# Performance work log

Measured on AMD Instinct MI355X. Metric: run time of the kernel, lower is better.

## Reference

```python
import jax, jax.numpy as jnp
import numpy as np

EPS = 1e-7  # keras K.epsilon()
ROUTINGS = 3


def squash(v, axis=-1):
    s = jnp.sum(v * v, axis=axis, keepdims=True)
    scale = s / (1.0 + s) / jnp.sqrt(s + EPS)
    return scale * v


def setup_inputs() -> dict:
    key = jax.random.key(0)
    k1, k2 = jax.random.split(key)
    B, I, K = 256, 2048, 8   # batch, input_num_capsule, input_dim_capsule
    J, D = 10, 16            # num_capsule, dim_capsule
    inputs = jax.random.normal(k1, (B, I, K), dtype=jnp.float32)
    W = jax.random.normal(k2, (J, I, D, K), dtype=jnp.float32) * 0.05
    return {"inputs": inputs, "W": W}


def reference(inputs, W):
    # inputs: [B, I, K]; W: [J, I, D, K]
    # inputs_hat[b,j,i,d] = W[j,i] @ inputs[b,i]  -> [B, J, I, D]
    u_hat = jnp.einsum('jidk,bik->bjid', W, inputs)
    B, J, I, _ = u_hat.shape
    b = jnp.zeros((B, J, 1, I), dtype=u_hat.dtype)
    outputs = None
    for r in range(ROUTINGS):
        c = jax.nn.softmax(b, axis=1)                       # softmax over output capsules
        s = jnp.einsum('bjqi,bjid->bjqd', c, u_hat)          # [B, J, 1, D]
        outputs = squash(s, axis=-1)
        if r < ROUTINGS - 1:
            b = b + jnp.einsum('bjqd,bjid->bjqi', outputs, u_hat)
    return jnp.squeeze(outputs, axis=2)                      # [B, J, D]
```

## Files before the change

### kernel.cpp

```cpp
#include <hip/hip_runtime.h>
#include <math.h>


#define BB 256
#define II 2048
#define KK 8
#define JJ 10
#define DD 16

typedef __attribute__((ext_vector_type(4))) float f32x4;
typedef __attribute__((ext_vector_type(8))) short short8;

__device__ __forceinline__ short f2bf(float f) {
    union { float f; unsigned u; } v; v.f = f;
    unsigned r = v.u + 0x7FFFu + ((v.u >> 16) & 1u);
    return (short)(r >> 16);
}

__global__ __launch_bounds__(256) void pre_kernel(const float* __restrict__ x,
                                                  const float* __restrict__ W,
                                                  short* __restrict__ xTb,
                                                  short* __restrict__ Wb) {
    __shared__ float4 tile[8 * 66];
    const int t = threadIdx.x;
    const int bid = blockIdx.x;
    if (bid < 1280) {
        const int idx = bid * 256 + t;
        const float4* src = (const float4*)(W + (size_t)idx * 8);
        const float4 a = src[0], b = src[1];
        short8 o;
        o[0] = f2bf(a.x); o[1] = f2bf(a.y); o[2] = f2bf(a.z); o[3] = f2bf(a.w);
        o[4] = f2bf(b.x); o[5] = f2bf(b.y); o[6] = f2bf(b.z); o[7] = f2bf(b.w);
        *(short8*)(Wb + (size_t)idx * 8) = o;
    } else {
        const int bb = bid - 1280;
        const int b0 = (bb >> 8) * 32, i0 = (bb & 255) * 8;
        {
            const int lb = t >> 3, li = t & 7;
            const float4* src = (const float4*)(x + ((b0 + lb) * II + (i0 + li)) * KK);
            tile[li * 66 + lb * 2 + 0] = src[0];
            tile[li * 66 + lb * 2 + 1] = src[1];
        }
        __syncthreads();
        {
            const int ri = t >> 5, rb = t & 31;
            const float4 p0 = tile[ri * 66 + rb * 2 + 0];
            const float4 p1 = tile[ri * 66 + rb * 2 + 1];
            short8 o;
            o[0] = f2bf(p0.x); o[1] = f2bf(p0.y); o[2] = f2bf(p0.z); o[3] = f2bf(p0.w);
            o[4] = f2bf(p1.x); o[5] = f2bf(p1.y); o[6] = f2bf(p1.z); o[7] = f2bf(p1.w);
            *(short8*)(xTb + ((size_t)(i0 + ri) * BB + (b0 + rb)) * KK) = o;
        }
    }
}

#define LBUF 14336

__device__ __forceinline__ void seg_src_dst(int s, int i0, int b0,
                                            const short* __restrict__ xTb,
                                            const short* __restrict__ Wb,
                                            const short** src, int* dst) {
    if (s < 20) {
        const int j = s >> 1, h = s & 1;
        *src = Wb + ((size_t)(j * II + i0) * DD) * KK + h * 512;
        *dst = j * 1024 + h * 512;
    } else {
        const int il = s - 20;
        *src = xTb + ((size_t)(i0 + il) * BB + b0) * KK;
        *dst = 10240 + il * 512;
    }
}

template <int USE_C>
__global__ __launch_bounds__(256) void round_mfma(
    const short* __restrict__ xTb, const short* __restrict__ Wb,
    const float* __restrict__ vT, _Float16* __restrict__ p)
{
    __shared__ short L[2][LBUF];
    const int t = threadIdx.x;
    const int lane = t & 63, wv = t >> 6;
    const int col = lane & 15, q = lane >> 4;
    const int bid = blockIdx.x;
    const int chunk = ((bid >> 5) << 3) | (bid & 7);
    const int ytile = (bid >> 3) & 3;
    const int b0 = ytile * 64;
    const int bl = wv * 16 + col;
    const int i0 = chunk * 16;

    short8 r0[7], r1[7];
#pragma unroll
    for (int n = 0; n < 7; ++n) {
        const int s = wv + n * 4;
        const short* src; int dst;
        seg_src_dst(s, i0, b0, xTb, Wb, &src, &dst);
        r0[n] = *(const short8*)(src + lane * 8);
        seg_src_dst(s, i0 + 8, b0, xTb, Wb, &src, &dst);
        r1[n] = *(const short8*)(src + lane * 8);
    }
#pragma unroll
    for (int n = 0; n < 7; ++n) {
        const int s = wv + n * 4;
        const short* src; int dst;
        seg_src_dst(s, i0, b0, xTb, Wb, &src, &dst);
        *(short8*)(&L[0][dst + lane * 8]) = r0[n];
    }
    __syncthreads();

    f32x4 sfrag[JJ];
#pragma unroll
    for (int j = 0; j < JJ; ++j) sfrag[j] = (f32x4){0.f, 0.f, 0.f, 0.f};

    f32x4 vfrag[JJ];
    if (USE_C) {
#pragma unroll
        for (int j = 0; j < JJ; ++j)
            vfrag[j] = *(const f32x4*)(vT + ((size_t)j * BB + b0 + bl) * DD + q * 4);
    }

#pragma unroll
    for (int sc = 0; sc < 2; ++sc) {
        const short* Lb = L[sc];
        if (USE_C) {
            for (int il = 0; il < 8; ++il) {
                short8 A[JJ], Bf;
                const short8 z = (short8){0, 0, 0, 0, 0, 0, 0, 0};
                Bf = z;
#pragma unroll
                for (int j = 0; j < JJ; ++j) A[j] = z;
                if (q == 0) {
                    Bf = *(const short8*)(&Lb[10240 + il * 512 + bl * 8]);
#pragma unroll
                    for (int j = 0; j < JJ; ++j)
                        A[j] = *(const short8*)(&Lb[j * 1024 + il * 128 + col * 8]);
                }
                f32x4 U[JJ];
#pragma unroll
                for (int j = 0; j < JJ; ++j)
                    U[j] = __builtin_amdgcn_mfma_f32_16x16x32_bf16(
                        A[j], Bf, (f32x4){0.f, 0.f, 0.f, 0.f}, 0, 0, 0);
                float Lg[JJ];
#pragma unroll
                for (int j = 0; j < JJ; ++j)
                    Lg[j] = vfrag[j][0] * U[j][0] + vfrag[j][1] * U[j][1]
                          + vfrag[j][2] * U[j][2] + vfrag[j][3] * U[j][3];
#pragma unroll
                for (int j = 0; j < JJ; ++j) {
                    Lg[j] += __shfl_xor(Lg[j], 16, 64);
                    Lg[j] += __shfl_xor(Lg[j], 32, 64);
                }
                float sum = 0.f;
#pragma unroll
                for (int j = 0; j < JJ; ++j) { Lg[j] = __expf(Lg[j]); sum += Lg[j]; }
                const float inv = __builtin_amdgcn_rcpf(sum);
#pragma unroll
                for (int j = 0; j < JJ; ++j) {
                    const float c = Lg[j] * inv;
#pragma unroll
                    for (int r = 0; r < 4; ++r) sfrag[j][r] += c * U[j][r];
                }
            }
        } else {
#pragma unroll
            for (int s = 0; s < 2; ++s) {
                const int il = s * 4 + q;
                const short8 Bf = *(const short8*)(&Lb[10240 + il * 512 + bl * 8]);
#pragma unroll
                for (int j = 0; j < JJ; ++j) {
                    const short8 A = *(const short8*)(&Lb[j * 1024 + il * 128 + col * 8]);
                    sfrag[j] = __builtin_amdgcn_mfma_f32_16x16x32_bf16(A, Bf, sfrag[j], 0, 0, 0);
                }
            }
        }
        if (sc == 0) {
#pragma unroll
            for (int n = 0; n < 7; ++n) {
                const int s = wv + n * 4;
                const short* src; int dst;
                seg_src_dst(s, i0 + 8, b0, xTb, Wb, &src, &dst);
                *(short8*)(&L[1][dst + lane * 8]) = r1[n];
            }
            __syncthreads();
        }
    }

    _Float16* pp = p + (((size_t)(ytile * 4 + wv) * 128 + chunk) * 5) * 512;
#pragma unroll
    for (int jp = 0; jp < 5; ++jp) {
        union { uint4 u; _Float16 h[8]; } pk;
        pk.h[0] = (_Float16)sfrag[2 * jp][0];
        pk.h[1] = (_Float16)sfrag[2 * jp][1];
        pk.h[2] = (_Float16)sfrag[2 * jp][2];
        pk.h[3] = (_Float16)sfrag[2 * jp][3];
        pk.h[4] = (_Float16)sfrag[2 * jp + 1][0];
        pk.h[5] = (_Float16)sfrag[2 * jp + 1][1];
        pk.h[6] = (_Float16)sfrag[2 * jp + 1][2];
        pk.h[7] = (_Float16)sfrag[2 * jp + 1][3];
        *(uint4*)(pp + (size_t)(jp * 64 + lane) * 8) = pk.u;
    }
}

template <int MODE>
__global__ __launch_bounds__(256) void rs_kernel(const _Float16* __restrict__ p,
                                                 float* __restrict__ vT,
                                                 float* __restrict__ out, float scale) {
    __shared__ float red[256][9];
    const int t = threadIdx.x;
    const int jp = blockIdx.x, bt = blockIdx.y;
    const int eg = t & 63, cg = t >> 6;

    const _Float16* pp = p + (((size_t)bt * 128 + cg * 32) * 5 + jp) * 512 + eg * 8;
    float s[8];
#pragma unroll
    for (int r = 0; r < 8; ++r) s[r] = 0.f;
#pragma unroll 4
    for (int ch = 0; ch < 32; ++ch) {
        union { uint4 u; _Float16 h[8]; } cv;
        cv.u = *(const uint4*)(pp + (size_t)ch * (5 * 512));
#pragma unroll
        for (int r = 0; r < 8; ++r) s[r] += (float)cv.h[r];
    }
#pragma unroll
    for (int r = 0; r < 8; ++r) red[t][r] = s[r];
    __syncthreads();
    if (t < 64) {
        float a[8];
#pragma unroll
        for (int r = 0; r < 8; ++r)
            a[r] = red[t][r] + red[t + 64][r] + red[t + 128][r] + red[t + 192][r];
        const int qd = t >> 4, bc = t & 15;
#pragma unroll
        for (int jj = 0; jj < 2; ++jj) {
            const int j = jp * 2 + jj;
            const float x0 = a[jj * 4 + 0] * scale, x1 = a[jj * 4 + 1] * scale;
            const float x2 = a[jj * 4 + 2] * scale, x3 = a[jj * 4 + 3] * scale;
            float ss = x0 * x0 + x1 * x1 + x2 * x2 + x3 * x3;
            ss += __shfl_xor(ss, 16, 64);
            ss += __shfl_xor(ss, 32, 64);
            const float coef = ss / (1.f + ss) / sqrtf(ss + 1e-7f);
            f32x4 v = {coef * x0, coef * x1, coef * x2, coef * x3};
            if (MODE == 0)
                *(f32x4*)(vT + ((size_t)j * BB + bt * 16 + bc) * DD + qd * 4) = v;
            if (MODE == 1) {
                f32x4 o = *(f32x4*)(vT + ((size_t)j * BB + bt * 16 + bc) * DD + qd * 4);
                o += v;
                *(f32x4*)(vT + ((size_t)j * BB + bt * 16 + bc) * DD + qd * 4) = o;
            }
            if (MODE == 2)
                *(f32x4*)(out + ((size_t)(bt * 16 + bc) * JJ + j) * DD + qd * 4) = v;
        }
    }
}

#define IT_OLD 32
#define BT_OLD 16

__global__ __launch_bounds__(256) void zero_kernel(float* __restrict__ p, int n) {
    int idx = blockIdx.x * blockDim.x + threadIdx.x;
    if (idx < n) p[idx] = 0.f;
}

__global__ __launch_bounds__(256) void squash_old(float* __restrict__ s_acc,
                                                  float* __restrict__ dst, float scale,
                                                  int add_to_dst, int zero_src) {
    int idx = blockIdx.x * blockDim.x + threadIdx.x;
    if (idx >= BB * JJ) return;
    float s[DD];
    float ss = 0.f;
#pragma unroll
    for (int d = 0; d < DD; ++d) {
        s[d] = s_acc[idx * DD + d] * scale;
        ss += s[d] * s[d];
    }
    const float coef = ss / (1.f + ss) / sqrtf(ss + 1e-7f);
#pragma unroll
    for (int d = 0; d < DD; ++d) {
        const float vv = coef * s[d];
        if (add_to_dst) dst[idx * DD + d] += vv;
        else            dst[idx * DD + d] = vv;
        if (zero_src)   s_acc[idx * DD + d] = 0.f;
    }
}

__global__ __launch_bounds__(256) void round1_old(const float* __restrict__ x,
                                                  const float* __restrict__ W,
                                                  float* __restrict__ s_acc) {
    const int t = threadIdx.x;
    const int d = t & 15;
    const int bq = t >> 4;
    const int b = blockIdx.y * BT_OLD + bq;
    const int i0 = blockIdx.x * IT_OLD;
    float acc[JJ];
#pragma unroll
    for (int j = 0; j < JJ; ++j) acc[j] = 0.f;
    for (int ii = 0; ii < IT_OLD; ++ii) {
        const int i = i0 + ii;
        const float* xp = x + ((b * II) + i) * KK;
        const float4 xa = *(const float4*)(xp);
        const float4 xb = *(const float4*)(xp + 4);
#pragma unroll
        for (int j = 0; j < JJ; ++j) {
            const float* wp = W + (((j * II + i) * DD + d) * KK);
            const float4 w0 = *(const float4*)(wp);
            const float4 w1 = *(const float4*)(wp + 4);
            acc[j] += w0.x*xa.x + w0.y*xa.y + w0.z*xa.z + w0.w*xa.w
                    + w1.x*xb.x + w1.y*xb.y + w1.z*xb.z + w1.w*xb.w;
        }
    }
#pragma unroll
    for (int j = 0; j < JJ; ++j)
        atomicAdd(&s_acc[(b * JJ + j) * DD + d], acc[j]);
}

__global__ __launch_bounds__(256) void round_old(const float* __restrict__ x,
                                                 const float* __restrict__ W,
                                                 const float* __restrict__ v,
                                                 float* __restrict__ s_acc) {
    const int t = threadIdx.x;
    const int d = t & 15;
    const int bq = t >> 4;
    const int b = blockIdx.y * BT_OLD + bq;
    const int i0 = blockIdx.x * IT_OLD;
    float vr[JJ], acc[JJ];
#pragma unroll
    for (int j = 0; j < JJ; ++j) {
        vr[j] = v[(b * JJ + j) * DD + d];
        acc[j] = 0.f;
    }
    for (int ii = 0; ii < IT_OLD; ++ii) {
        const int i = i0 + ii;
        const float* xp = x + ((b * II) + i) * KK;
        const float4 xa = *(const float4*)(xp);
        const float4 xb = *(const float4*)(xp + 4);
        float U[JJ], Lg[JJ];
#pragma unroll
        for (int j = 0; j < JJ; ++j) {
            const float* wp = W + (((j * II + i) * DD + d) * KK);
            const float4 w0 = *(const float4*)(wp);
            const float4 w1 = *(const float4*)(wp + 4);
            U[j] = w0.x*xa.x + w0.y*xa.y + w0.z*xa.z + w0.w*xa.w
                 + w1.x*xb.x + w1.y*xb.y + w1.z*xb.z + w1.w*xb.w;
            Lg[j] = vr[j] * U[j];
        }
#pragma unroll
        for (int m = 8; m >= 1; m >>= 1) {
#pragma unroll
            for (int j = 0; j < JJ; ++j) Lg[j] += __shfl_xor(Lg[j], m, 64);
        }
        float mx = Lg[0];
#pragma unroll
        for (int j = 1; j < JJ; ++j) mx = fmaxf(mx, Lg[j]);
        float sum = 0.f;
#pragma unroll
        for (int j = 0; j < JJ; ++j) { Lg[j] = __expf(Lg[j] - mx); sum += Lg[j]; }
        const float inv = 1.f / sum;
#pragma unroll
        for (int j = 0; j < JJ; ++j) acc[j] += (Lg[j] * inv) * U[j];
    }
#pragma unroll
    for (int j = 0; j < JJ; ++j)
        atomicAdd(&s_acc[(b * JJ + j) * DD + d], acc[j]);
}

extern "C" void kernel_launch(void* const* d_in, const int* in_sizes, int n_in,
                              void* d_out, int out_size, void* d_ws, size_t ws_size,
                              hipStream_t stream) {
    const float* x = (const float*)d_in[0];
    const float* W = (const float*)d_in[1];
    float* out = (float*)d_out;

    float* vT     = (float*)d_ws;
    _Float16* p   = (_Float16*)(vT + BB * JJ * DD);
    short* xTb    = (short*)(p + (size_t)16 * 128 * 2560);
    short* Wb     = xTb + (size_t)II * BB * KK;
    const size_t need = (size_t)(BB * JJ * DD) * 4
                      + (size_t)16 * 128 * 2560 * 2
                      + ((size_t)II * BB * KK + (size_t)JJ * II * DD * KK) * 2;

    if (ws_size >= need) {
        pre_kernel<<<1280 + 2048, 256, 0, stream>>>(x, W, xTb, Wb);

        dim3 sg(5, 16);
        round_mfma<0><<<512, 256, 0, stream>>>(xTb, Wb, vT, p);
        rs_kernel<0><<<sg, 256, 0, stream>>>(p, vT, out, 0.1f);
        round_mfma<1><<<512, 256, 0, stream>>>(xTb, Wb, vT, p);
        rs_kernel<1><<<sg, 256, 0, stream>>>(p, vT, out, 1.0f);
        round_mfma<1><<<512, 256, 0, stream>>>(xTb, Wb, vT, p);
        rs_kernel<2><<<sg, 256, 0, stream>>>(p, vT, out, 1.0f);
    } else {
        float* s_acc = (float*)d_ws;
        float* v_buf = s_acc + BB * JJ * DD;
        const int NS = BB * JJ * DD;
        dim3 rg(II / IT_OLD, BB / BT_OLD);
        zero_kernel<<<(NS + 255) / 256, 256, 0, stream>>>(s_acc, NS);
        round1_old<<<rg, 256, 0, stream>>>(x, W, s_acc);
        squash_old<<<(BB * JJ + 255) / 256, 256, 0, stream>>>(s_acc, v_buf, 0.1f, 0, 1);
        round_old<<<rg, 256, 0, stream>>>(x, W, v_buf, s_acc);
        squash_old<<<(BB * JJ + 255) / 256, 256, 0, stream>>>(s_acc, v_buf, 1.0f, 1, 1);
        round_old<<<rg, 256, 0, stream>>>(x, W, v_buf, s_acc);
        squash_old<<<(BB * JJ + 255) / 256, 256, 0, stream>>>(s_acc, out, 1.0f, 0, 0);
    }
}
```

Baseline: 146.2 us.

## Fuse preprocessing and all routing rounds into one cooperative kernel with grid syncs

Replaces the seven separate launches (bf16 conversion, three MFMA routing rounds, three reduce/squash passes) with a single cooperative kernel of 512 blocks that uses grid.sync between phases. The goal is to remove launch gaps and kernel-boundary drains between the short dependent stages. In exchange it needs all 512 blocks co-resident, which is why launch_bounds asks for 2 blocks per CU. The reduce/squash phase runs on only 80 blocks while the rest wait at the barrier, and the block-to-tile mapping changes from the swizzled layout. If the cooperative launch fails, the code falls back to the old multi-kernel path.

```diff
diff --git a/kernel.cpp b/kernel.cpp
--- a/kernel.cpp
+++ b/kernel.cpp
@@ -1,5 +1,8 @@
 #include <hip/hip_runtime.h>
+#include <hip/hip_cooperative_groups.h>
 #include <math.h>
+
+namespace cg = cooperative_groups;
 
 
 #define BB 256
@@ -16,6 +19,261 @@
     unsigned r = v.u + 0x7FFFu + ((v.u >> 16) & 1u);
     return (short)(r >> 16);
 }
+
+#define LBUF 14336
+
+__device__ __forceinline__ void seg_src_dst(int s, int i0, int b0,
+                                            const short* __restrict__ xTb,
+                                            const short* __restrict__ Wb,
+                                            const short** src, int* dst) {
+    if (s < 20) {
+        const int j = s >> 1, h = s & 1;
+        *src = Wb + ((size_t)(j * II + i0) * DD) * KK + h * 512;
+        *dst = j * 1024 + h * 512;
+    } else {
+        const int il = s - 20;
+        *src = xTb + ((size_t)(i0 + il) * BB + b0) * KK;
+        *dst = 10240 + il * 512;
+    }
+}
+
+__global__ __launch_bounds__(256, 2) void fused_all(
+    const float* __restrict__ x, const float* __restrict__ W,
+    short* __restrict__ xTb, short* __restrict__ Wb,
+    float* __restrict__ vT, _Float16* __restrict__ p, float* __restrict__ out)
+{
+    __shared__ short L[2][LBUF];
+    cg::grid_group grid = cg::this_grid();
+    const int t = threadIdx.x;
+    const int bid = blockIdx.x;
+
+    for (int u = bid; u < 3328; u += 512) {
+        if (u < 1280) {
+            const int idx = u * 256 + t;
+            const float4* src = (const float4*)(W + (size_t)idx * 8);
+            const float4 a = src[0], b = src[1];
+            short8 o;
+            o[0] = f2bf(a.x); o[1] = f2bf(a.y); o[2] = f2bf(a.z); o[3] = f2bf(a.w);
+            o[4] = f2bf(b.x); o[5] = f2bf(b.y); o[6] = f2bf(b.z); o[7] = f2bf(b.w);
+            *(short8*)(Wb + (size_t)idx * 8) = o;
+        } else {
+            float4* tile = (float4*)(&L[0][0]);
+            const int bb = u - 1280;
+            const int b0p = (bb >> 8) * 32, i0p = (bb & 255) * 8;
+            __syncthreads();
+            {
+                const int lb = t >> 3, li = t & 7;
+                const float4* src = (const float4*)(x + ((b0p + lb) * II + (i0p + li)) * KK);
+                tile[li * 66 + lb * 2 + 0] = src[0];
+                tile[li * 66 + lb * 2 + 1] = src[1];
+            }
+            __syncthreads();
+            {
+                const int ri = t >> 5, rb = t & 31;
+                const float4 p0 = tile[ri * 66 + rb * 2 + 0];
+                const float4 p1 = tile[ri * 66 + rb * 2 + 1];
+                short8 o;
+                o[0] = f2bf(p0.x); o[1] = f2bf(p0.y); o[2] = f2bf(p0.z); o[3] = f2bf(p0.w);
+                o[4] = f2bf(p1.x); o[5] = f2bf(p1.y); o[6] = f2bf(p1.z); o[7] = f2bf(p1.w);
+                *(short8*)(xTb + ((size_t)(i0p + ri) * BB + (b0p + rb)) * KK) = o;
+            }
+        }
+    }
+    grid.sync();
+
+    const int lane = t & 63, wv = t >> 6;
+    const int col = lane & 15, q = lane >> 4;
+    const int chunk = bid & 127;
+    const int ytile = (bid >> 7) & 3;
+    const int b0 = ytile * 64;
+    const int bl = wv * 16 + col;
+    const int i0 = chunk * 16;
+
+    short8 r0[7], r1[7];
+#pragma unroll
+    for (int n = 0; n < 7; ++n) {
+        const int s = wv + n * 4;
+        const short* src; int dst;
+        seg_src_dst(s, i0, b0, xTb, Wb, &src, &dst);
+        r0[n] = *(const short8*)(src + lane * 8);
+        seg_src_dst(s, i0 + 8, b0, xTb, Wb, &src, &dst);
+        r1[n] = *(const short8*)(src + lane * 8);
+    }
+#pragma unroll
+    for (int n = 0; n < 7; ++n) {
+        const int s = wv + n * 4;
+        const short* src; int dst;
+        seg_src_dst(s, i0, b0, xTb, Wb, &src, &dst);
+        *(short8*)(&L[0][dst + lane * 8]) = r0[n];
+    }
+    __syncthreads();
+
+#pragma unroll 1
+    for (int r = 0; r < 3; ++r) {
+        f32x4 sfrag[JJ];
+#pragma unroll
+        for (int j = 0; j < JJ; ++j) sfrag[j] = (f32x4){0.f, 0.f, 0.f, 0.f};
+
+        f32x4 vfrag[JJ];
+        if (r > 0) {
+#pragma unroll
+            for (int j = 0; j < JJ; ++j)
+                vfrag[j] = *(const f32x4*)(vT + ((size_t)j * BB + b0 + bl) * DD + q * 4);
+        }
+
+#pragma unroll
+        for (int sc = 0; sc < 2; ++sc) {
+            const short* Lb = L[sc];
+            if (r > 0) {
+                for (int il = 0; il < 8; ++il) {
+                    short8 A[JJ], Bf;
+                    const short8 z = (short8){0, 0, 0, 0, 0, 0, 0, 0};
+                    Bf = z;
+#pragma unroll
+                    for (int j = 0; j < JJ; ++j) A[j] = z;
+                    if (q == 0) {
+                        Bf = *(const short8*)(&Lb[10240 + il * 512 + bl * 8]);
+#pragma unroll
+                        for (int j = 0; j < JJ; ++j)
+                            A[j] = *(const short8*)(&Lb[j * 1024 + il * 128 + col * 8]);
+                    }
+                    f32x4 U[JJ];
+#pragma unroll
+                    for (int j = 0; j < JJ; ++j)
+                        U[j] = __builtin_amdgcn_mfma_f32_16x16x32_bf16(
+                            A[j], Bf, (f32x4){0.f, 0.f, 0.f, 0.f}, 0, 0, 0);
+                    float Lg[JJ];
+#pragma unroll
+                    for (int j = 0; j < JJ; ++j)
+                        Lg[j] = vfrag[j][0] * U[j][0] + vfrag[j][1] * U[j][1]
+                              + vfrag[j][2] * U[j][2] + vfrag[j][3] * U[j][3];
+#pragma unroll
+                    for (int j = 0; j < JJ; ++j) {
+                        Lg[j] += __shfl_xor(Lg[j], 16, 64);
+                        Lg[j] += __shfl_xor(Lg[j], 32, 64);
+                    }
+                    float sum = 0.f;
+#pragma unroll
+                    for (int j = 0; j < JJ; ++j) { Lg[j] = __expf(Lg[j]); sum += Lg[j]; }
+                    const float inv = __builtin_amdgcn_rcpf(sum);
+#pragma unroll
+                    for (int j = 0; j < JJ; ++j) {
+                        const float c = Lg[j] * inv;
+#pragma unroll
+                        for (int rr = 0; rr < 4; ++rr) sfrag[j][rr] += c * U[j][rr];
+                    }
+                }
+            } else {
+#pragma unroll
+                for (int s = 0; s < 2; ++s) {
+                    const int il = s * 4 + q;
+                    const short8 Bf = *(const short8*)(&Lb[10240 + il * 512 + bl * 8]);
+#pragma unroll
+                    for (int j = 0; j < JJ; ++j) {
+                        const short8 A = *(const short8*)(&Lb[j * 1024 + il * 128 + col * 8]);
+                        sfrag[j] = __builtin_amdgcn_mfma_f32_16x16x32_bf16(A, Bf, sfrag[j], 0, 0, 0);
+                    }
+                }
+            }
+            if (sc == 0) {
+#pragma unroll
+                for (int n = 0; n < 7; ++n) {
+                    const int s = wv + n * 4;
+                    const short* src; int dst;
+                    seg_src_dst(s, i0 + 8, b0, xTb, Wb, &src, &dst);
+                    *(short8*)(&L[1][dst + lane * 8]) = r1[n];
+                }
+                __syncthreads();
+            }
+        }
+
+        _Float16* pp = p + (((size_t)(ytile * 4 + wv) * 128 + chunk) * 5) * 512;
+#pragma unroll
+        for (int jp = 0; jp < 5; ++jp) {
+            union { uint4 u; _Float16 h[8]; } pk;
+            pk.h[0] = (_Float16)sfrag[2 * jp][0];
+            pk.h[1] = (_Float16)sfrag[2 * jp][1];
+            pk.h[2] = (_Float16)sfrag[2 * jp][2];
+            pk.h[3] = (_Float16)sfrag[2 * jp][3];
+            pk.h[4] = (_Float16)sfrag[2 * jp + 1][0];
+            pk.h[5] = (_Float16)sfrag[2 * jp + 1][1];
+            pk.h[6] = (_Float16)sfrag[2 * jp + 1][2];
+            pk.h[7] = (_Float16)sfrag[2 * jp + 1][3];
+            *(uint4*)(pp + (size_t)(jp * 64 + lane) * 8) = pk.u;
+        }
+
+        if (r < 2) {
+#pragma unroll
+            for (int n = 0; n < 7; ++n) {
+                const int s = wv + n * 4;
+                const short* src; int dst;
+                seg_src_dst(s, i0, b0, xTb, Wb, &src, &dst);
+                r0[n] = *(const short8*)(src + lane * 8);
+                seg_src_dst(s, i0 + 8, b0, xTb, Wb, &src, &dst);
+                r1[n] = *(const short8*)(src + lane * 8);
+            }
+#pragma unroll
+            for (int n = 0; n < 7; ++n) {
+                const int s = wv + n * 4;
+                const short* src; int dst;
+                seg_src_dst(s, i0, b0, xTb, Wb, &src, &dst);
+                *(short8*)(&L[0][dst + lane * 8]) = r0[n];
+            }
+        }
+
+        grid.sync();
+
+        if (bid < 80) {
+            const int jp = bid % 5, btq = bid / 5;
+            const int eg = t & 63, cgi = t >> 6;
+            float (*red)[9] = (float (*)[9])(&L[1][0]);
+            const _Float16* prd = p + (((size_t)btq * 128 + cgi * 32) * 5 + jp) * 512 + eg * 8;
+            float sacc[8];
+#pragma unroll
+            for (int rr = 0; rr < 8; ++rr) sacc[rr] = 0.f;
+#pragma unroll 4
+            for (int ch = 0; ch < 32; ++ch) {
+                union { uint4 u; _Float16 h[8]; } cv;
+                cv.u = *(const uint4*)(prd + (size_t)ch * (5 * 512));
+#pragma unroll
+                for (int rr = 0; rr < 8; ++rr) sacc[rr] += (float)cv.h[rr];
+            }
+#pragma unroll
+            for (int rr = 0; rr < 8; ++rr) red[t][rr] = sacc[rr];
+            __syncthreads();
+            if (t < 64) {
+                float a[8];
+#pragma unroll
+                for (int rr = 0; rr < 8; ++rr)
+                    a[rr] = red[t][rr] + red[t + 64][rr] + red[t + 128][rr] + red[t + 192][rr];
+                const int qd = t >> 4, bc = t & 15;
+                const float scale = (r == 0) ? 0.1f : 1.0f;
+#pragma unroll
+                for (int jj = 0; jj < 2; ++jj) {
+                    const int j = jp * 2 + jj;
+                    const float x0 = a[jj * 4 + 0] * scale, x1 = a[jj * 4 + 1] * scale;
+                    const float x2 = a[jj * 4 + 2] * scale, x3 = a[jj * 4 + 3] * scale;
+                    float ss = x0 * x0 + x1 * x1 + x2 * x2 + x3 * x3;
+                    ss += __shfl_xor(ss, 16, 64);
+                    ss += __shfl_xor(ss, 32, 64);
+                    const float coef = ss / (1.f + ss) / sqrtf(ss + 1e-7f);
+                    f32x4 v = {coef * x0, coef * x1, coef * x2, coef * x3};
+                    if (r == 0)
+                        *(f32x4*)(vT + ((size_t)j * BB + btq * 16 + bc) * DD + qd * 4) = v;
+                    else if (r == 1) {
+                        f32x4 o = *(f32x4*)(vT + ((size_t)j * BB + btq * 16 + bc) * DD + qd * 4);
+                        o += v;
+                        *(f32x4*)(vT + ((size_t)j * BB + btq * 16 + bc) * DD + qd * 4) = o;
+                    } else
+                        *(f32x4*)(out + ((size_t)(btq * 16 + bc) * JJ + j) * DD + qd * 4) = v;
+                }
+            }
+        }
+
+        if (r < 2) grid.sync();
+    }
+}
+
 
 __global__ __launch_bounds__(256) void pre_kernel(const float* __restrict__ x,
                                                   const float* __restrict__ W,
@@ -54,23 +312,6 @@
     }
 }
 
-#define LBUF 14336
-
-__device__ __forceinline__ void seg_src_dst(int s, int i0, int b0,
-                                            const short* __restrict__ xTb,
-                                            const short* __restrict__ Wb,
-                                            const short** src, int* dst) {
-    if (s < 20) {
-        const int j = s >> 1, h = s & 1;
-        *src = Wb + ((size_t)(j * II + i0) * DD) * KK + h * 512;
-        *dst = j * 1024 + h * 512;
-    } else {
-        const int il = s - 20;
-        *src = xTb + ((size_t)(i0 + il) * BB + b0) * KK;
-        *dst = 10240 + il * 512;
-    }
-}
-
 template <int USE_C>
 __global__ __launch_bounds__(256) void round_mfma(
     const short* __restrict__ xTb, const short* __restrict__ Wb,
@@ -80,9 +321,8 @@
     const int t = threadIdx.x;
     const int lane = t & 63, wv = t >> 6;
     const int col = lane & 15, q = lane >> 4;
-    const int bid = blockIdx.x;
-    const int chunk = ((bid >> 5) << 3) | (bid & 7);
-    const int ytile = (bid >> 3) & 3;
+    const int chunk = blockIdx.x;
+    const int ytile = blockIdx.y;
     const int b0 = ytile * 64;
     const int bl = wv * 16 + col;
     const int i0 = chunk * 16;
@@ -156,7 +396,7 @@
                 for (int j = 0; j < JJ; ++j) {
                     const float c = Lg[j] * inv;
 #pragma unroll
-                    for (int r = 0; r < 4; ++r) sfrag[j][r] += c * U[j][r];
+                    for (int rr = 0; rr < 4; ++rr) sfrag[j][rr] += c * U[j][rr];
                 }
             }
         } else {
@@ -206,27 +446,27 @@
     __shared__ float red[256][9];
     const int t = threadIdx.x;
     const int jp = blockIdx.x, bt = blockIdx.y;
-    const int eg = t & 63, cg = t >> 6;
-
-    const _Float16* pp = p + (((size_t)bt * 128 + cg * 32) * 5 + jp) * 512 + eg * 8;
+    const int eg = t & 63, cgi = t >> 6;
+
+    const _Float16* pp = p + (((size_t)bt * 128 + cgi * 32) * 5 + jp) * 512 + eg * 8;
     float s[8];
 #pragma unroll
-    for (int r = 0; r < 8; ++r) s[r] = 0.f;
+    for (int rr = 0; rr < 8; ++rr) s[rr] = 0.f;
 #pragma unroll 4
     for (int ch = 0; ch < 32; ++ch) {
         union { uint4 u; _Float16 h[8]; } cv;
         cv.u = *(const uint4*)(pp + (size_t)ch * (5 * 512));
 #pragma unroll
-        for (int r = 0; r < 8; ++r) s[r] += (float)cv.h[r];
-    }
-#pragma unroll
-    for (int r = 0; r < 8; ++r) red[t][r] = s[r];
+        for (int rr = 0; rr < 8; ++rr) s[rr] += (float)cv.h[rr];
+    }
+#pragma unroll
+    for (int rr = 0; rr < 8; ++rr) red[t][rr] = s[rr];
     __syncthreads();
     if (t < 64) {
         float a[8];
 #pragma unroll
-        for (int r = 0; r < 8; ++r)
-            a[r] = red[t][r] + red[t + 64][r] + red[t + 128][r] + red[t + 192][r];
+        for (int rr = 0; rr < 8; ++rr)
+            a[rr] = red[t][rr] + red[t + 64][rr] + red[t + 128][rr] + red[t + 192][rr];
         const int qd = t >> 4, bc = t & 15;
 #pragma unroll
         for (int jj = 0; jj < 2; ++jj) {
@@ -377,15 +617,25 @@
                       + ((size_t)II * BB * KK + (size_t)JJ * II * DD * KK) * 2;
 
     if (ws_size >= need) {
-        pre_kernel<<<1280 + 2048, 256, 0, stream>>>(x, W, xTb, Wb);
-
-        dim3 sg(5, 16);
-        round_mfma<0><<<512, 256, 0, stream>>>(xTb, Wb, vT, p);
-        rs_kernel<0><<<sg, 256, 0, stream>>>(p, vT, out, 0.1f);
-        round_mfma<1><<<512, 256, 0, stream>>>(xTb, Wb, vT, p);
-        rs_kernel<1><<<sg, 256, 0, stream>>>(p, vT, out, 1.0f);
-        round_mfma<1><<<512, 256, 0, stream>>>(xTb, Wb, vT, p);
-        rs_kernel<2><<<sg, 256, 0, stream>>>(p, vT, out, 1.0f);
+        const float* xa = x; const float* Wa = W;
+        short* xta = xTb; short* Wba = Wb;
+        float* vta = vT; _Float16* pa = p; float* oa = out;
+        void* ka[7] = {(void*)&xa, (void*)&Wa, (void*)&xta, (void*)&Wba,
+                       (void*)&vta, (void*)&pa, (void*)&oa};
+        hipError_t e = hipLaunchCooperativeKernel((const void*)fused_all,
+                                                  dim3(512), dim3(256), ka, 0, stream);
+        if (e != hipSuccess) {
+            (void)hipGetLastError();
+            pre_kernel<<<1280 + 2048, 256, 0, stream>>>(x, W, xTb, Wb);
+            dim3 rg(128, 4);
+            dim3 sg(5, 16);
+            round_mfma<0><<<rg, 256, 0, stream>>>(xTb, Wb, vT, p);
+            rs_kernel<0><<<sg, 256, 0, stream>>>(p, vT, out, 0.1f);
+            round_mfma<1><<<rg, 256, 0, stream>>>(xTb, Wb, vT, p);
+            rs_kernel<1><<<sg, 256, 0, stream>>>(p, vT, out, 1.0f);
+            round_mfma<1><<<rg, 256, 0, stream>>>(xTb, Wb, vT, p);
+            rs_kernel<2><<<sg, 256, 0, stream>>>(p, vT, out, 1.0f);
+        }
     } else {
         float* s_acc = (float*)d_ws;
         float* v_buf = s_acc + BB * JJ * DD;
```

After: 507.5 us. 247% more time.

## Halve per-block input chunk to double routing grid and widen reduction blocks

Applied to the files above, without the earlier changes.

The routing kernel now gives each block 8 input capsules instead of 16, which drops the second LDS buffer and the staged prefetch. The launch becomes a 2D grid of 256x4 blocks instead of 512 blocks, doubling the number of blocks to improve occupancy and latency hiding. The partial-sum buffer doubles in size. The reduce/squash kernel now uses 512 threads so it can sum twice as many partials, which adds global traffic and reduction work per round.

```diff
diff --git a/kernel.cpp b/kernel.cpp
--- a/kernel.cpp
+++ b/kernel.cpp
@@ -7,6 +7,7 @@
 #define KK 8
 #define JJ 10
 #define DD 16
+#define CH 256
 
 typedef __attribute__((ext_vector_type(4))) float f32x4;
 typedef __attribute__((ext_vector_type(8))) short short8;
@@ -76,33 +77,30 @@
     const short* __restrict__ xTb, const short* __restrict__ Wb,
     const float* __restrict__ vT, _Float16* __restrict__ p)
 {
-    __shared__ short L[2][LBUF];
+    __shared__ short L[LBUF];
     const int t = threadIdx.x;
     const int lane = t & 63, wv = t >> 6;
     const int col = lane & 15, q = lane >> 4;
-    const int bid = blockIdx.x;
-    const int chunk = ((bid >> 5) << 3) | (bid & 7);
-    const int ytile = (bid >> 3) & 3;
+    const int chunk = blockIdx.x;
+    const int ytile = blockIdx.y;
     const int b0 = ytile * 64;
     const int bl = wv * 16 + col;
-    const int i0 = chunk * 16;
-
-    short8 r0[7], r1[7];
+    const int i0 = chunk * 8;
+
+    short8 r0[7];
 #pragma unroll
     for (int n = 0; n < 7; ++n) {
         const int s = wv + n * 4;
         const short* src; int dst;
         seg_src_dst(s, i0, b0, xTb, Wb, &src, &dst);
         r0[n] = *(const short8*)(src + lane * 8);
-        seg_src_dst(s, i0 + 8, b0, xTb, Wb, &src, &dst);
-        r1[n] = *(const short8*)(src + lane * 8);
     }
 #pragma unroll
     for (int n = 0; n < 7; ++n) {
         const int s = wv + n * 4;
         const short* src; int dst;
         seg_src_dst(s, i0, b0, xTb, Wb, &src, &dst);
-        *(short8*)(&L[0][dst + lane * 8]) = r0[n];
+        *(short8*)(&L[dst + lane * 8]) = r0[n];
     }
     __syncthreads();
 
@@ -110,80 +108,64 @@
 #pragma unroll
     for (int j = 0; j < JJ; ++j) sfrag[j] = (f32x4){0.f, 0.f, 0.f, 0.f};
 
-    f32x4 vfrag[JJ];
     if (USE_C) {
+        f32x4 vfrag[JJ];
 #pragma unroll
         for (int j = 0; j < JJ; ++j)
             vfrag[j] = *(const f32x4*)(vT + ((size_t)j * BB + b0 + bl) * DD + q * 4);
-    }
-
-#pragma unroll
-    for (int sc = 0; sc < 2; ++sc) {
-        const short* Lb = L[sc];
-        if (USE_C) {
-            for (int il = 0; il < 8; ++il) {
-                short8 A[JJ], Bf;
-                const short8 z = (short8){0, 0, 0, 0, 0, 0, 0, 0};
-                Bf = z;
-#pragma unroll
-                for (int j = 0; j < JJ; ++j) A[j] = z;
-                if (q == 0) {
-                    Bf = *(const short8*)(&Lb[10240 + il * 512 + bl * 8]);
-#pragma unroll
-                    for (int j = 0; j < JJ; ++j)
-                        A[j] = *(const short8*)(&Lb[j * 1024 + il * 128 + col * 8]);
-                }
-                f32x4 U[JJ];
+
+        for (int il = 0; il < 8; ++il) {
+            short8 A[JJ], Bf;
+            const short8 z = (short8){0, 0, 0, 0, 0, 0, 0, 0};
+            Bf = z;
+#pragma unroll
+            for (int j = 0; j < JJ; ++j) A[j] = z;
+            if (q == 0) {
+                Bf = *(const short8*)(&L[10240 + il * 512 + bl * 8]);
 #pragma unroll
                 for (int j = 0; j < JJ; ++j)
-                    U[j] = __builtin_amdgcn_mfma_f32_16x16x32_bf16(
-                        A[j], Bf, (f32x4){0.f, 0.f, 0.f, 0.f}, 0, 0, 0);
-                float Lg[JJ];
-#pragma unroll
-                for (int j = 0; j < JJ; ++j)
-                    Lg[j] = vfrag[j][0] * U[j][0] + vfrag[j][1] * U[j][1]
-                          + vfrag[j][2] * U[j][2] + vfrag[j][3] * U[j][3];
-#pragma unroll
-                for (int j = 0; j < JJ; ++j) {
-                    Lg[j] += __shfl_xor(Lg[j], 16, 64);
-                    Lg[j] += __shfl_xor(Lg[j], 32, 64);
-                }
-                float sum = 0.f;
-#pragma unroll
-                for (int j = 0; j < JJ; ++j) { Lg[j] = __expf(Lg[j]); sum += Lg[j]; }
-                const float inv = __builtin_amdgcn_rcpf(sum);
-#pragma unroll
-                for (int j = 0; j < JJ; ++j) {
-                    const float c = Lg[j] * inv;
-#pragma unroll
-                    for (int r = 0; r < 4; ++r) sfrag[j][r] += c * U[j][r];
-                }
-            }
-        } else {
-#pragma unroll
-            for (int s = 0; s < 2; ++s) {
-                const int il = s * 4 + q;
-                const short8 Bf = *(const short8*)(&Lb[10240 + il * 512 + bl * 8]);
-#pragma unroll
-                for (int j = 0; j < JJ; ++j) {
-                    const short8 A = *(const short8*)(&Lb[j * 1024 + il * 128 + col * 8]);
-                    sfrag[j] = __builtin_amdgcn_mfma_f32_16x16x32_bf16(A, Bf, sfrag[j], 0, 0, 0);
-                }
-            }
-        }
-        if (sc == 0) {
-#pragma unroll
-            for (int n = 0; n < 7; ++n) {
-                const int s = wv + n * 4;
-                const short* src; int dst;
-                seg_src_dst(s, i0 + 8, b0, xTb, Wb, &src, &dst);
-                *(short8*)(&L[1][dst + lane * 8]) = r1[n];
-            }
-            __syncthreads();
-        }
-    }
-
-    _Float16* pp = p + (((size_t)(ytile * 4 + wv) * 128 + chunk) * 5) * 512;
+                    A[j] = *(const short8*)(&L[j * 1024 + il * 128 + col * 8]);
+            }
+            f32x4 U[JJ];
+#pragma unroll
+            for (int j = 0; j < JJ; ++j)
+                U[j] = __builtin_amdgcn_mfma_f32_16x16x32_bf16(
+                    A[j], Bf, (f32x4){0.f, 0.f, 0.f, 0.f}, 0, 0, 0);
+            float Lg[JJ];
+#pragma unroll
+            for (int j = 0; j < JJ; ++j)
+                Lg[j] = vfrag[j][0] * U[j][0] + vfrag[j][1] * U[j][1]
+                      + vfrag[j][2] * U[j][2] + vfrag[j][3] * U[j][3];
+#pragma unroll
+            for (int j = 0; j < JJ; ++j) {
+                Lg[j] += __shfl_xor(Lg[j], 16, 64);
+                Lg[j] += __shfl_xor(Lg[j], 32, 64);
+            }
+            float sum = 0.f;
+#pragma unroll
+            for (int j = 0; j < JJ; ++j) { Lg[j] = __expf(Lg[j]); sum += Lg[j]; }
+            const float inv = __builtin_amdgcn_rcpf(sum);
+#pragma unroll
+            for (int j = 0; j < JJ; ++j) {
+                const float c = Lg[j] * inv;
+#pragma unroll
+                for (int r = 0; r < 4; ++r) sfrag[j][r] += c * U[j][r];
+            }
+        }
+    } else {
+#pragma unroll
+        for (int s = 0; s < 2; ++s) {
+            const int il = s * 4 + q;
+            const short8 Bf = *(const short8*)(&L[10240 + il * 512 + bl * 8]);
+#pragma unroll
+            for (int j = 0; j < JJ; ++j) {
+                const short8 A = *(const short8*)(&L[j * 1024 + il * 128 + col * 8]);
+                sfrag[j] = __builtin_amdgcn_mfma_f32_16x16x32_bf16(A, Bf, sfrag[j], 0, 0, 0);
+            }
+        }
+    }
+
+    _Float16* pp = p + (((size_t)(ytile * 4 + wv) * CH + chunk) * 5) * 512;
 #pragma unroll
     for (int jp = 0; jp < 5; ++jp) {
         union { uint4 u; _Float16 h[8]; } pk;
@@ -200,19 +182,19 @@
 }
 
 template <int MODE>
-__global__ __launch_bounds__(256) void rs_kernel(const _Float16* __restrict__ p,
+__global__ __launch_bounds__(512) void rs_kernel(const _Float16* __restrict__ p,
                                                  float* __restrict__ vT,
                                                  float* __restrict__ out, float scale) {
-    __shared__ float red[256][9];
+    __shared__ float red[512][9];
     const int t = threadIdx.x;
     const int jp = blockIdx.x, bt = blockIdx.y;
     const int eg = t & 63, cg = t >> 6;
 
-    const _Float16* pp = p + (((size_t)bt * 128 + cg * 32) * 5 + jp) * 512 + eg * 8;
+    const _Float16* pp = p + (((size_t)bt * CH + cg * 32) * 5 + jp) * 512 + eg * 8;
     float s[8];
 #pragma unroll
     for (int r = 0; r < 8; ++r) s[r] = 0.f;
-#pragma unroll 4
+#pragma unroll 8
     for (int ch = 0; ch < 32; ++ch) {
         union { uint4 u; _Float16 h[8]; } cv;
         cv.u = *(const uint4*)(pp + (size_t)ch * (5 * 512));
@@ -225,8 +207,12 @@
     if (t < 64) {
         float a[8];
 #pragma unroll
-        for (int r = 0; r < 8; ++r)
-            a[r] = red[t][r] + red[t + 64][r] + red[t + 128][r] + red[t + 192][r];
+        for (int r = 0; r < 8; ++r) {
+            float acc = red[t][r];
+#pragma unroll
+            for (int g = 1; g < 8; ++g) acc += red[t + 64 * g][r];
+            a[r] = acc;
+        }
         const int qd = t >> 4, bc = t & 15;
 #pragma unroll
         for (int jj = 0; jj < 2; ++jj) {
@@ -370,22 +356,23 @@
 
     float* vT     = (float*)d_ws;
     _Float16* p   = (_Float16*)(vT + BB * JJ * DD);
-    short* xTb    = (short*)(p + (size_t)16 * 128 * 2560);
+    short* xTb    = (short*)(p + (size_t)16 * CH * 2560);
     short* Wb     = xTb + (size_t)II * BB * KK;
     const size_t need = (size_t)(BB * JJ * DD) * 4
-                      + (size_t)16 * 128 * 2560 * 2
+                      + (size_t)16 * CH * 2560 * 2
                       + ((size_t)II * BB * KK + (size_t)JJ * II * DD * KK) * 2;
 
     if (ws_size >= need) {
         pre_kernel<<<1280 + 2048, 256, 0, stream>>>(x, W, xTb, Wb);
 
+        dim3 rg(CH, 4);
         dim3 sg(5, 16);
-        round_mfma<0><<<512, 256, 0, stream>>>(xTb, Wb, vT, p);
-        rs_kernel<0><<<sg, 256, 0, stream>>>(p, vT, out, 0.1f);
-        round_mfma<1><<<512, 256, 0, stream>>>(xTb, Wb, vT, p);
-        rs_kernel<1><<<sg, 256, 0, stream>>>(p, vT, out, 1.0f);
-        round_mfma<1><<<512, 256, 0, stream>>>(xTb, Wb, vT, p);
-        rs_kernel<2><<<sg, 256, 0, stream>>>(p, vT, out, 1.0f);
+        round_mfma<0><<<rg, 256, 0, stream>>>(xTb, Wb, vT, p);
+        rs_kernel<0><<<sg, 512, 0, stream>>>(p, vT, out, 0.1f);
+        round_mfma<1><<<rg, 256, 0, stream>>>(xTb, Wb, vT, p);
+        rs_kernel<1><<<sg, 512, 0, stream>>>(p, vT, out, 1.0f);
+        round_mfma<1><<<rg, 256, 0, stream>>>(xTb, Wb, vT, p);
+        rs_kernel<2><<<sg, 512, 0, stream>>>(p, vT, out, 1.0f);
     } else {
         float* s_acc = (float*)d_ws;
         float* v_buf = s_acc + BB * JJ * DD;
```

Result: no change. 144.6 us (-1.1%).
